# Kernel optimization log

Measured on AMD Instinct MI355X. Metric: run time of the kernel, lower is better.

## Reference

```python
import jax, jax.numpy as jnp
import numpy as np

B, N, C = 1, 2048, 64


def setup_inputs() -> dict:
    key = jax.random.key(0)
    ks = jax.random.split(key, 7)
    X = jax.random.normal(ks[0], (B, N, 3), jnp.float32)
    embs = jax.random.normal(ks[1], (B, N, C), jnp.float32)
    w0 = jax.random.uniform(ks[2], (N,), jnp.float32)
    s0 = jax.random.uniform(ks[3], (N,), jnp.float32)
    paired_mask = jax.random.uniform(ks[4], (B, N, N), jnp.float32)
    # params: xavier_uniform(gain=0.1) + 1.0  ->  ~1.0 with small spread
    depth_factor = 1.0 + 0.05 * jax.random.normal(ks[5], (2 * C, 1), jnp.float32)
    radius_factor = 1.0 + 0.05 * jax.random.normal(ks[6], (2 * C, 1), jnp.float32)
    return {"X": X, "embs": embs, "w0": w0, "s0": s0, "paired_mask": paired_mask,
            "depth_factor": depth_factor, "radius_factor": radius_factor}


def reference(X, embs, w0, s0, paired_mask, depth_factor, radius_factor):
    c = embs.shape[-1]
    # pairwise distances; torch adds 1e-6 per coordinate before the sum
    V = X[:, None, :, :] - X[:, :, None, :]            # (B,N,N,3), V[b,i,j] = X[b,j]-X[b,i]
    D = jnp.sqrt(jnp.sum(V * V + 1e-6, axis=-1))       # (B,N,N)

    # emb_ij[b,i,j] = concat(embs[b,j], embs[b,i]); matmul with (2C,1) factor
    # splits exactly into two per-node dot products broadcast over the pair grid,
    # so the (B,N,N,2C) concat tensor never needs to be materialized.
    sig_r = jax.nn.sigmoid(embs @ radius_factor[c:, 0][:, None] .squeeze(-1)[:, :, None]
                           + (embs @ radius_factor[:c, 0][:, None]).squeeze(-1)[:, None, :]) if False else \
        jax.nn.sigmoid(jnp.einsum('bnc,c->bn', embs, radius_factor[c:, 0])[:, :, None]
                       + jnp.einsum('bnc,c->bn', embs, radius_factor[:c, 0])[:, None, :])  # (B,N,N)
    sig_d = jax.nn.sigmoid(jnp.einsum('bnc,c->bn', embs, depth_factor[c:, 0])[:, :, None]
                           + jnp.einsum('bnc,c->bn', embs, depth_factor[:c, 0])[:, None, :])  # (B,N,N)

    s0_ij = (s0[None, :] + s0[:, None])[None, None]    # (1,1,N,N)
    s = s0_ij * (0.8 * sig_r + 0.4)                    # (B,B(=1),N,N)

    repl = 5.0 * jnp.exp(-0.3 * D * D * D) * paired_mask   # (B,N,N)

    Dm = D - s                                          # (1,1,N,N) via broadcast
    attr = (jnp.exp(-(Dm - 0.3) * (Dm - 0.3))
            + jnp.exp(-3.0 * Dm * Dm)
            + jnp.exp(-10.0 * Dm * Dm)) / 3.0 * paired_mask

    w0_ij = jnp.sqrt(w0[None, :] * w0[:, None] + 1e-6)[None, None]  # (1,1,N,N)
    w = w0_ij * (sig_d + 0.5)

    Etotal = jnp.sum(-w * attr + repl[None])            # scalar
    Etotal = jnp.where(jnp.isnan(Etotal), jnp.float32(1e-6), Etotal)
    return Etotal
```

## Files before the change

### kernel.cpp

```cpp
#include <hip/hip_runtime.h>

#define NN 2048
#define CC 64

__global__ void node_dots_kernel(const float* __restrict__ embs,
                                 const float* __restrict__ depth_factor,
                                 const float* __restrict__ radius_factor,
                                 float* __restrict__ ws) {
    int node = (blockIdx.x * blockDim.x + threadIdx.x) >> 6;
    int lane = threadIdx.x & 63;
    if (node >= NN) return;

    float e  = embs[node * CC + lane];
    float rl = e * radius_factor[lane];
    float rh = e * radius_factor[CC + lane];
    float dl = e * depth_factor[lane];
    float dh = e * depth_factor[CC + lane];

    #pragma unroll
    for (int off = 32; off > 0; off >>= 1) {
        rl += __shfl_down(rl, off, 64);
        rh += __shfl_down(rh, off, 64);
        dl += __shfl_down(dl, off, 64);
        dh += __shfl_down(dh, off, 64);
    }
    if (lane == 0) {
        ws[node]          = rl;
        ws[NN + node]     = rh;
        ws[2 * NN + node] = dl;
        ws[3 * NN + node] = dh;
    }
}

__global__ void pair_energy_kernel(const float* __restrict__ X,
                                   const float* __restrict__ w0,
                                   const float* __restrict__ s0,
                                   const float* __restrict__ mask,
                                   const float* __restrict__ ws,
                                   float* __restrict__ out) {
    const float* __restrict__ r_lo = ws;
    const float* __restrict__ r_hi = ws + NN;
    const float* __restrict__ d_lo = ws + 2 * NN;
    const float* __restrict__ d_hi = ws + 3 * NN;

    const int i = blockIdx.x;
    const float xi  = X[3 * i];
    const float yi  = X[3 * i + 1];
    const float zi  = X[3 * i + 2];
    const float rhi = r_hi[i];
    const float dhi = d_hi[i];
    const float s0i = s0[i];
    const float w0i = w0[i];

    float acc = 0.0f;
    const float* mrow = mask + (size_t)i * NN;

    for (int j = threadIdx.x; j < NN; j += blockDim.x) {
        float dx = X[3 * j]     - xi;
        float dy = X[3 * j + 1] - yi;
        float dz = X[3 * j + 2] - zi;
        float d2 = dx * dx + dy * dy + dz * dz + 3e-6f;
        float D  = __builtin_amdgcn_sqrtf(d2);

        float er    = __expf(-(rhi + r_lo[j]));
        float sig_r = __builtin_amdgcn_rcpf(1.0f + er);
        float ed    = __expf(-(dhi + d_lo[j]));
        float sig_d = __builtin_amdgcn_rcpf(1.0f + ed);

        float m = mrow[j];

        float s  = (s0i + s0[j]) * (0.8f * sig_r + 0.4f);
        float Dm = D - s;
        float t  = Dm - 0.3f;

        float repl = 5.0f * __expf(-0.3f * d2 * D) * m;
        float attr = (__expf(-t * t)
                    + __expf(-3.0f * Dm * Dm)
                    + __expf(-10.0f * Dm * Dm)) * (1.0f / 3.0f) * m;

        float w = __builtin_amdgcn_sqrtf(w0i * w0[j] + 1e-6f) * (sig_d + 0.5f);

        acc += repl - w * attr;
    }

    #pragma unroll
    for (int off = 32; off > 0; off >>= 1) acc += __shfl_down(acc, off, 64);

    __shared__ float red[4];
    int lane = threadIdx.x & 63;
    int wid  = threadIdx.x >> 6;
    if (lane == 0) red[wid] = acc;
    __syncthreads();
    if (threadIdx.x == 0) {
        float v = red[0] + red[1] + red[2] + red[3];
        atomicAdd(out, v);
    }
}

extern "C" void kernel_launch(void* const* d_in, const int* in_sizes, int n_in,
                              void* d_out, int out_size, void* d_ws, size_t ws_size,
                              hipStream_t stream) {
    const float* X             = (const float*)d_in[0];
    const float* embs          = (const float*)d_in[1];
    const float* w0            = (const float*)d_in[2];
    const float* s0            = (const float*)d_in[3];
    const float* paired_mask   = (const float*)d_in[4];
    const float* depth_factor  = (const float*)d_in[5];
    const float* radius_factor = (const float*)d_in[6];

    float* out = (float*)d_out;
    float* ws  = (float*)d_ws;

    hipMemsetAsync(out, 0, sizeof(float), stream);

    node_dots_kernel<<<dim3(NN / 4), dim3(256), 0, stream>>>(
        embs, depth_factor, radius_factor, ws);

    pair_energy_kernel<<<dim3(NN), dim3(256), 0, stream>>>(
        X, w0, s0, paired_mask, ws, out);
}
```

Baseline: 106.9 us.

## Pack per-node data, vectorize mask loads, and cut exps via power identities

Result: no change. 105.4 us (-1.5%).

```diff
diff --git a/kernel.cpp b/kernel.cpp
--- a/kernel.cpp
+++ b/kernel.cpp
@@ -3,11 +3,18 @@
 #define NN 2048
 #define CC 64
 
-__global__ void node_dots_kernel(const float* __restrict__ embs,
-                                 const float* __restrict__ depth_factor,
-                                 const float* __restrict__ radius_factor,
-                                 float* __restrict__ ws) {
-    int node = (blockIdx.x * blockDim.x + threadIdx.x) >> 6;
+__global__ void prep_kernel(const float* __restrict__ embs,
+                            const float* __restrict__ depth_factor,
+                            const float* __restrict__ radius_factor,
+                            const float* __restrict__ s0,
+                            const float* __restrict__ w0,
+                            float4* __restrict__ pj,
+                            float* __restrict__ ih,
+                            float* __restrict__ out) {
+    int gid = blockIdx.x * blockDim.x + threadIdx.x;
+    if (gid == 0) out[0] = 0.0f;
+
+    int node = gid >> 6;
     int lane = threadIdx.x & 63;
     if (node >= NN) return;
 
@@ -25,62 +32,77 @@
         dh += __shfl_down(dh, off, 64);
     }
     if (lane == 0) {
-        ws[node]          = rl;
-        ws[NN + node]     = rh;
-        ws[2 * NN + node] = dl;
-        ws[3 * NN + node] = dh;
+        pj[node] = make_float4(rl, dl, s0[node], w0[node]);
+        ih[node]      = rh;
+        ih[NN + node] = dh;
     }
 }
 
-__global__ void pair_energy_kernel(const float* __restrict__ X,
-                                   const float* __restrict__ w0,
-                                   const float* __restrict__ s0,
-                                   const float* __restrict__ mask,
-                                   const float* __restrict__ ws,
-                                   float* __restrict__ out) {
-    const float* __restrict__ r_lo = ws;
-    const float* __restrict__ r_hi = ws + NN;
-    const float* __restrict__ d_lo = ws + 2 * NN;
-    const float* __restrict__ d_hi = ws + 3 * NN;
+__device__ __forceinline__ float pair_e(float xj, float yj, float zj,
+                                        float4 p, float m,
+                                        float xi, float yi, float zi,
+                                        float rhi, float dhi,
+                                        float s0i, float w0i) {
+    float dx = xj - xi, dy = yj - yi, dz = zj - zi;
+    float d2 = fmaf(dx, dx, fmaf(dy, dy, fmaf(dz, dz, 3e-6f)));
+    float D  = __builtin_amdgcn_sqrtf(d2);
 
+    float sig_r = __builtin_amdgcn_rcpf(1.0f + __expf(-(rhi + p.x)));
+    float sig_d = __builtin_amdgcn_rcpf(1.0f + __expf(-(dhi + p.y)));
+
+    float s  = (s0i + p.z) * fmaf(0.8f, sig_r, 0.4f);
+    float Dm = D - s;
+
+    float repl = 5.0f * __expf(-0.3f * d2 * D);
+
+    float e1 = __expf(-Dm * Dm);
+    float g  = __expf(fmaf(0.6f, Dm, -0.09f));
+    float e2 = e1 * e1;
+    float e4 = e2 * e2;
+    float e8 = e4 * e4;
+    float attr3 = fmaf(e1, g, e2 * e1) + e8 * e2;
+
+    float w = __builtin_amdgcn_sqrtf(fmaf(w0i, p.w, 1e-6f)) * (sig_d + 0.5f);
+
+    return m * fmaf(-w * (1.0f / 3.0f), attr3, repl);
+}
+
+__global__ __launch_bounds__(256) void pair_energy_kernel(
+        const float* __restrict__ X,
+        const float* __restrict__ mask,
+        const float4* __restrict__ pj,
+        const float* __restrict__ ih,
+        float* __restrict__ out) {
     const int i = blockIdx.x;
     const float xi  = X[3 * i];
     const float yi  = X[3 * i + 1];
     const float zi  = X[3 * i + 2];
-    const float rhi = r_hi[i];
-    const float dhi = d_hi[i];
-    const float s0i = s0[i];
-    const float w0i = w0[i];
+    const float rhi = ih[i];
+    const float dhi = ih[NN + i];
+    const float4 pi = pj[i];
+    const float s0i = pi.z;
+    const float w0i = pi.w;
+
+    const float4* __restrict__ mrow = (const float4*)(mask + (size_t)i * NN);
+    const float4* __restrict__ X4   = (const float4*)X;
 
     float acc = 0.0f;
-    const float* mrow = mask + (size_t)i * NN;
+    #pragma unroll
+    for (int it = 0; it < NN / (4 * 256); ++it) {
+        int j4 = threadIdx.x + it * 256;
+        float4 m  = mrow[j4];
+        float4 xa = X4[3 * j4];
+        float4 xb = X4[3 * j4 + 1];
+        float4 xc = X4[3 * j4 + 2];
+        float4 p0 = pj[4 * j4];
+        float4 p1 = pj[4 * j4 + 1];
+        float4 p2 = pj[4 * j4 + 2];
+        float4 p3 = pj[4 * j4 + 3];
 
-    for (int j = threadIdx.x; j < NN; j += blockDim.x) {
-        float dx = X[3 * j]     - xi;
-        float dy = X[3 * j + 1] - yi;
-        float dz = X[3 * j + 2] - zi;
-        float d2 = dx * dx + dy * dy + dz * dz + 3e-6f;
-        float D  = __builtin_amdgcn_sqrtf(d2);
-
-        float er    = __expf(-(rhi + r_lo[j]));
-        float sig_r = __builtin_amdgcn_rcpf(1.0f + er);
-        float ed    = __expf(-(dhi + d_lo[j]));
-        float sig_d = __builtin_amdgcn_rcpf(1.0f + ed);
-
-        float m = mrow[j];
-
-        float s  = (s0i + s0[j]) * (0.8f * sig_r + 0.4f);
-        float Dm = D - s;
-        float t  = Dm - 0.3f;
-
-        float repl = 5.0f * __expf(-0.3f * d2 * D) * m;
-        float attr = (__expf(-t * t)
-                    + __expf(-3.0f * Dm * Dm)
-                    + __expf(-10.0f * Dm * Dm)) * (1.0f / 3.0f) * m;
-
-        float w = __builtin_amdgcn_sqrtf(w0i * w0[j] + 1e-6f) * (sig_d + 0.5f);
-
-        acc += repl - w * attr;
+        acc += pair_e(xa.x, xa.y, xa.z, p0, m.x, xi, yi, zi, rhi, dhi, s0i, w0i);
+        acc += pair_e(xa.w, xb.x, xb.y, p1, m.y, xi, yi, zi, rhi, dhi, s0i, w0i);
+        acc += pair_e(xb.z, xb.w, xc.x, p2, m.z, xi, yi, zi, rhi, dhi, s0i, w0i);
+        acc += pair_e(xc.y, xc.z, xc.w, p3, m.w, xi, yi, zi, rhi, dhi, s0i, w0i);
     }
 
     #pragma unroll
@@ -92,8 +114,7 @@
     if (lane == 0) red[wid] = acc;
     __syncthreads();
     if (threadIdx.x == 0) {
-        float v = red[0] + red[1] + red[2] + red[3];
-        atomicAdd(out, v);
+        atomicAdd(out, red[0] + red[1] + red[2] + red[3]);
     }
 }
 
@@ -108,14 +129,13 @@
     const float* depth_factor  = (const float*)d_in[5];
     const float* radius_factor = (const float*)d_in[6];
 
-    float* out = (float*)d_out;
-    float* ws  = (float*)d_ws;
+    float*  out = (float*)d_out;
+    float4* pj  = (float4*)d_ws;
+    float*  ih  = (float*)d_ws + 4 * NN;
 
-    hipMemsetAsync(out, 0, sizeof(float), stream);
-
-    node_dots_kernel<<<dim3(NN / 4), dim3(256), 0, stream>>>(
-        embs, depth_factor, radius_factor, ws);
+    prep_kernel<<<dim3(NN / 4), dim3(256), 0, stream>>>(
+        embs, depth_factor, radius_factor, s0, w0, pj, ih, out);
 
     pair_energy_kernel<<<dim3(NN), dim3(256), 0, stream>>>(
-        X, w0, s0, paired_mask, ws, out);
+        X, paired_mask, pj, ih, out);
 }
```
